# Kernel tuning notes

Hardware: AMD Instinct MI355X
Metric: run time of the kernel (lower is better)

The kernel has to match this reference:

```python
import jax, jax.numpy as jnp
import numpy as np

NB, NLOC, NALL, NNEI, A_SEL = 1, 512, 640, 96, 20
N_DIM, E_DIM, A_DIM, AXIS = 128, 64, 64, 4
EDGE_INFO = 2 * N_DIM + E_DIM          # 320
SYM = AXIS * (E_DIM + N_DIM)           # 768, cal_1_dim
ANGLE = A_DIM + N_DIM + 2 * E_DIM      # 320, angle_dim


def setup_inputs() -> dict:
    key = jax.random.key(0)
    ks = jax.random.split(key, 16)
    nrm = lambda k, sh, s=1.0: jax.random.normal(k, sh, dtype=jnp.float32) * s

    def lin(k, din, dout, s=0.05):
        k1, k2 = jax.random.split(k)
        return nrm(k1, (din, dout), s), nrm(k2, (dout,), s)

    inp = {}
    inp["g1_ext"] = nrm(ks[0], (NB, NALL, N_DIM))
    inp["g2"] = nrm(ks[1], (NB, NLOC, NNEI, E_DIM))
    inp["h2"] = nrm(ks[2], (NB, NLOC, NNEI, 3))
    inp["angle_embed"] = nrm(ks[3], (NB, NLOC, A_SEL, A_SEL, A_DIM))
    inp["sw"] = jax.random.uniform(ks[4], (NB, NLOC, NNEI), dtype=jnp.float32)
    inp["a_sw"] = jax.random.uniform(ks[5], (NB, NLOC, A_SEL), dtype=jnp.float32)
    inp["w_self"], inp["b_self"] = lin(ks[6], N_DIM, N_DIM)
    inp["w_proj"] = nrm(ks[7], (E_DIM, N_DIM), 0.05)  # proj_g1g2, bias=False
    inp["w_lin1"], inp["b_lin1"] = lin(ks[8], SYM, N_DIM)
    inp["w_edge1"], inp["b_edge1"] = lin(ks[9], EDGE_INFO, N_DIM)
    inp["w_lin2"], inp["b_lin2"] = lin(ks[10], EDGE_INFO, E_DIM)
    inp["w_ang"], inp["b_ang"] = lin(ks[11], ANGLE, A_DIM)
    inp["w_ga1"], inp["b_ga1"] = lin(ks[12], ANGLE, E_DIM)
    inp["w_ga2"], inp["b_ga2"] = lin(ks[13], E_DIM, E_DIM)
    inp["nlist"] = jax.random.randint(ks[14], (NB, NLOC, NNEI), 0, NALL)
    inp["nlist_mask"] = jnp.ones((NB, NLOC, NNEI), dtype=bool)
    inp["a_nlist_mask"] = jnp.ones((NB, NLOC, A_SEL), dtype=bool)
    return inp


def _sym_op(g, h2, mask, sw, axis):
    # symmetrization_op: _cal_hg (smooth, use_sqrt_nnei) followed by _cal_grrg
    # g: nb x nloc x nnei x d, h2: nb x nloc x nnei x 3
    g = jnp.where(mask[..., None], g, 0.0) * sw[..., None]
    inv = np.float32(1.0 / np.sqrt(g.shape[2]))
    hg = jnp.einsum('blnt,blnd->bltd', h2, g) * inv
    grrg = jnp.einsum('bltd,blta->blda', hg, hg[..., :axis])  # nb x nloc x d x axis
    return grrg.reshape(grrg.shape[0], grrg.shape[1], -1)


def reference(g1_ext, g2, h2, angle_embed, sw, a_sw,
              w_self, b_self, w_proj, w_lin1, b_lin1, w_edge1, b_edge1,
              w_lin2, b_lin2, w_ang, b_ang, w_ga1, b_ga1, w_ga2, b_ga2,
              nlist, nlist_mask, a_nlist_mask):
    act = jax.nn.silu
    nb, nloc, nnei, e_dim = g2.shape
    n_dim = g1_ext.shape[-1]
    a_sel = angle_embed.shape[2]
    g1 = g1_ext[:, :nloc]
    # _make_nei_g1: gather neighbor node features, nb x nloc x nnei x n_dim
    gg1 = jnp.take_along_axis(
        g1_ext, nlist.reshape(nb, nloc * nnei, 1), axis=1
    ).reshape(nb, nloc, nnei, n_dim)
    maskf = nlist_mask[..., None]
    swf = sw[..., None]

    g1_update = [g1]
    # node self mlp
    g1_update.append(act(g1 @ w_self + b_self))
    # conv update: masked+switched gg1 times projected g2, mean over nnei
    gg1_ms = jnp.where(maskf, gg1, 0.0) * swf
    g1_update.append(jnp.sum((g2 @ w_proj) * gg1_ms, axis=2) / np.float32(nnei))
    # symmetrized axis-neuron update
    sym = jnp.concatenate(
        [_sym_op(g2, h2, nlist_mask, sw, AXIS),
         _sym_op(gg1, h2, nlist_mask, sw, AXIS)], axis=-1)
    g1_update.append(act(sym @ w_lin1 + b_lin1))
    # edge info: [tiled g1, gg1, g2] -> 2*n_dim + e_dim
    edge_info = jnp.concatenate(
        [jnp.broadcast_to(g1[:, :, None, :], (nb, nloc, nnei, n_dim)), gg1, g2],
        axis=-1)
    g1_edge = act(edge_info @ w_edge1 + b_edge1) * swf
    g1_update.append(jnp.sum(g1_edge, axis=2) / np.float32(nnei))
    # res_avg
    g1_new = sum(g1_update) / np.float32(np.sqrt(len(g1_update)))

    g2_update = [g2, act(edge_info @ w_lin2 + b_lin2)]

    # angle branch: angle_dim = a_dim + n_dim + 2*e_dim
    g2a = jnp.where(a_nlist_mask[..., None], g2[:, :, :a_sel, :], 0.0)
    ang = jnp.concatenate([
        angle_embed,
        jnp.broadcast_to(g1[:, :, None, None, :], (nb, nloc, a_sel, a_sel, n_dim)),
        jnp.broadcast_to(g2a[:, :, :, None, :], (nb, nloc, a_sel, a_sel, e_dim)),
        jnp.broadcast_to(g2a[:, :, None, :, :], (nb, nloc, a_sel, a_sel, e_dim)),
    ], axis=-1)
    a_new = (angle_embed + act(ang @ w_ang + b_ang)) / np.float32(np.sqrt(2.0))

    # angle -> edge message, switch-weighted on both angle axes, mean over one axis
    ang_w = ang * a_sw[:, :, :, None, None] * a_sw[:, :, None, :, None]
    g2_ang = jnp.sum(act(ang_w @ w_ga1 + b_ga1), axis=3) / np.float32(a_sel)
    g2_ang_full = jnp.concatenate(
        [g2_ang, jnp.zeros((nb, nloc, nnei - a_sel, e_dim), g2.dtype)], axis=2)
    g2_update.append(act(g2_ang_full @ w_ga2 + b_ga2))
    g2_new = sum(g2_update) / np.float32(np.sqrt(len(g2_update)))

    return g1_new, g2_new, h2, a_new
```

## Files before the change

kernel.cpp:

```cpp
#include <hip/hip_runtime.h>
#include <hip/hip_bf16.h>

#define NLOC 512
#define NALL 640
#define NNEI 96
#define ASEL 20
#define NDIM 128
#define EDIM 64
#define ADIM 64

typedef short bf16x8 __attribute__((ext_vector_type(8)));
typedef float f32x4 __attribute__((ext_vector_type(4)));
typedef unsigned short ushort8 __attribute__((ext_vector_type(8)));
typedef unsigned short ushort4_t __attribute__((ext_vector_type(4)));

__device__ __forceinline__ unsigned short f2bf(float f) {
    unsigned int u = __float_as_uint(f);
    unsigned int r = (u + 0x7FFFu + ((u >> 16) & 1u)) >> 16;
    return (unsigned short)r;
}
__device__ __forceinline__ float bf2f(unsigned short u) {
    return __uint_as_float(((unsigned int)u) << 16);
}
__device__ __forceinline__ float silu(float x) { return x / (1.0f + __expf(-x)); }

__device__ __forceinline__ void cvt8_store(unsigned short* dst, const float* src) {
    float4 f0 = *(const float4*)src;
    float4 f1 = *(const float4*)(src + 4);
    ushort8 v;
    v[0] = f2bf(f0.x); v[1] = f2bf(f0.y); v[2] = f2bf(f0.z); v[3] = f2bf(f0.w);
    v[4] = f2bf(f1.x); v[5] = f2bf(f1.y); v[6] = f2bf(f1.z); v[7] = f2bf(f1.w);
    *(ushort8*)dst = v;
}

__global__ void prep_bt2(const float* __restrict__ w_ang, const float* __restrict__ w_ga1,
                         const float* __restrict__ w_edge1, const float* __restrict__ w_lin2,
                         const float* __restrict__ w_proj, const float* __restrict__ w_self,
                         unsigned short* __restrict__ bt_ae, unsigned short* __restrict__ bt_g2e,
                         unsigned short* __restrict__ bt_sm, unsigned short* __restrict__ bt_pij) {
    int idx = blockIdx.x * 256 + threadIdx.x;
    if (idx < 8192) {
        int k = idx & 63, n = idx >> 6;
        bt_ae[idx] = f2bf((n < 64) ? w_ang[k * 64 + n] : w_ga1[k * 64 + (n - 64)]);
    } else if (idx < 32768) {
        int id2 = idx - 8192;
        int k = id2 & 63, n = id2 >> 6;
        float v;
        if (n < 128)      v = w_edge1[(256 + k) * 128 + n];
        else if (n < 192) v = w_lin2[(256 + k) * 64 + (n - 128)];
        else if (n < 256) v = 0.0f;
        else              v = w_proj[k * 128 + (n - 256)];
        bt_g2e[id2] = f2bf(v);
    } else if (idx < 114688) {
        int id3 = idx - 32768;
        int k = id3 & 127, n = id3 >> 7;
        float v;
        if (n < 128)      v = w_edge1[k * 128 + n];
        else if (n < 192) v = w_lin2[k * 64 + (n - 128)];
        else if (n < 320) v = w_edge1[(128 + k) * 128 + (n - 192)];
        else if (n < 384) v = w_lin2[(128 + k) * 64 + (n - 320)];
        else if (n < 512) { int c = n - 384;
            v = (c < 64) ? w_ang[(64 + k) * 64 + c] : w_ga1[(64 + k) * 64 + (c - 64)]; }
        else              v = w_self[k * 128 + (n - 512)];
        bt_sm[id3] = f2bf(v);
    } else {
        int id4 = idx - 114688;
        int k = id4 & 63, n = id4 >> 6;
        float v;
        if (n < 128) v = (n < 64) ? w_ang[(192 + k) * 64 + n] : w_ga1[(192 + k) * 64 + (n - 64)];
        else { int c = n - 128;
            v = (c < 64) ? w_ang[(256 + k) * 64 + c] : w_ga1[(256 + k) * 64 + (c - 64)]; }
        bt_pij[id4] = f2bf(v);
    }
}

__global__ __launch_bounds__(256) void gemm_small(
    const float* __restrict__ g1_ext, const unsigned short* __restrict__ bt_sm,
    const float* __restrict__ b_self, float* __restrict__ P1a, float* __restrict__ g1self,
    float* __restrict__ E1, float* __restrict__ E2) {
    const int m0 = blockIdx.x * 128;
    const int ntile = blockIdx.y;
    __shared__ __align__(16) unsigned short Asl[128 * 136];
    __shared__ __align__(16) unsigned short Bsl[128 * 136];
    const int tid = threadIdx.x;
#pragma unroll
    for (int u = 0; u < 8; u++) {
        int g = tid + u * 256;
        int row = g >> 4, seg = g & 15;
        cvt8_store(&Asl[row * 136 + seg * 8], g1_ext + (m0 + row) * 128 + seg * 8);
        *(ushort8*)&Bsl[row * 136 + seg * 8] =
            *(const ushort8*)&bt_sm[(ntile * 128 + row) * 128 + seg * 8];
    }
    __syncthreads();
    const int lane = tid & 63, wid = tid >> 6;
    const int wr = wid >> 1, wc = wid & 1;
    const int r15 = lane & 15, kg = lane >> 4;
    f32x4 acc[4][4] = {};
#pragma unroll
    for (int h = 0; h < 4; h++) {
        bf16x8 afr[4], bfr[4];
#pragma unroll
        for (int mi = 0; mi < 4; mi++)
            afr[mi] = *(const bf16x8*)&Asl[(wr * 64 + mi * 16 + r15) * 136 + h * 32 + kg * 8];
#pragma unroll
        for (int ni = 0; ni < 4; ni++)
            bfr[ni] = *(const bf16x8*)&Bsl[(wc * 64 + ni * 16 + r15) * 136 + h * 32 + kg * 8];
#pragma unroll
        for (int mi = 0; mi < 4; mi++)
#pragma unroll
            for (int ni = 0; ni < 4; ni++)
                acc[mi][ni] = __builtin_amdgcn_mfma_f32_16x16x32_bf16(afr[mi], bfr[ni], acc[mi][ni], 0, 0, 0);
    }
#pragma unroll
    for (int mi = 0; mi < 4; mi++) {
        int rbase = m0 + wr * 64 + mi * 16 + kg * 4;
#pragma unroll
        for (int ni = 0; ni < 4; ni++) {
            int gc = ntile * 128 + wc * 64 + ni * 16 + r15;
#pragma unroll
            for (int t2 = 0; t2 < 4; t2++) {
                int a = rbase + t2;
                float z = acc[mi][ni][t2];
                if (gc < 192) { if (a < 512) E1[a * 192 + gc] = z; }
                else if (gc < 384) E2[a * 192 + (gc - 192)] = z;
                else if (gc < 512) { if (a < 512) P1a[a * 128 + (gc - 384)] = z; }
                else { if (a < 512) g1self[a * 128 + (gc - 512)] = silu(z + b_self[gc - 512]); }
            }
        }
    }
}

__global__ __launch_bounds__(256) void gemm_pij(
    const float* __restrict__ g2, const unsigned short* __restrict__ bt_pij,
    unsigned short* __restrict__ P_i, unsigned short* __restrict__ P_j) {
    const int m0 = blockIdx.x * 128;
    const int ntile = blockIdx.y;
    __shared__ __align__(16) unsigned short Asl[128 * 72];
    const int tid = threadIdx.x;
#pragma unroll
    for (int u = 0; u < 4; u++) {
        int g = tid + u * 256;
        int row = g >> 3, seg = g & 7;
        int li = m0 + row, l = li / 20, i = li - l * 20;
        cvt8_store(&Asl[row * 72 + seg * 8], g2 + (l * 96 + i) * 64 + seg * 8);
    }
    __syncthreads();
    const int lane = tid & 63, wid = tid >> 6;
    const int wr = wid >> 1, wc = wid & 1;
    const int r15 = lane & 15, kg = lane >> 4;
    f32x4 acc[4][4] = {};
#pragma unroll
    for (int h = 0; h < 2; h++) {
        bf16x8 afr[4], bfr[4];
#pragma unroll
        for (int mi = 0; mi < 4; mi++)
            afr[mi] = *(const bf16x8*)&Asl[(wr * 64 + mi * 16 + r15) * 72 + h * 32 + kg * 8];
#pragma unroll
        for (int ni = 0; ni < 4; ni++)
            bfr[ni] = *(const bf16x8*)&bt_pij[(ntile * 128 + wc * 64 + ni * 16 + r15) * 64 + h * 32 + kg * 8];
#pragma unroll
        for (int mi = 0; mi < 4; mi++)
#pragma unroll
            for (int ni = 0; ni < 4; ni++)
                acc[mi][ni] = __builtin_amdgcn_mfma_f32_16x16x32_bf16(afr[mi], bfr[ni], acc[mi][ni], 0, 0, 0);
    }
    unsigned short* Pout = (ntile == 0) ? P_i : P_j;
#pragma unroll
    for (int mi = 0; mi < 4; mi++) {
        int rbase = m0 + wr * 64 + mi * 16 + kg * 4;
#pragma unroll
        for (int ni = 0; ni < 4; ni++) {
            int c = wc * 64 + ni * 16 + r15;
#pragma unroll
            for (int t2 = 0; t2 < 4; t2++)
                Pout[(rbase + t2) * 128 + c] = f2bf(acc[mi][ni][t2]);
        }
    }
}

__global__ void k_sym(const float* __restrict__ g1_ext, const float* __restrict__ g2,
                      const float* __restrict__ h2, const float* __restrict__ sw,
                      const int* __restrict__ nlist, const float* __restrict__ w_lin1,
                      const float* __restrict__ b_lin1, float* __restrict__ term4) {
    int l = blockIdx.x, t = threadIdx.x;
    __shared__ float h2s[96 * 3];
    __shared__ float sws[96];
    __shared__ int nls[96];
    __shared__ float hg[3 * 192];
    __shared__ float symv[768];
    __shared__ float red[128];
    if (t < 96) { sws[t] = sw[l * 96 + t]; nls[t] = nlist[l * 96 + t]; }
    for (int p = t; p < 288; p += 256) h2s[p] = h2[l * 288 + p];
    __syncthreads();
    const float inv = 0.1020620726f;
    for (int p = t; p < 576; p += 256) {
        float acc = 0.0f;
        if (p < 192) {
            int tt = p >> 6, d = p & 63;
            for (int n = 0; n < 96; n++)
                acc += h2s[n * 3 + tt] * g2[(l * 96 + n) * 64 + d] * sws[n];
            hg[tt * 192 + d] = acc * inv;
        } else {
            int q = p - 192;
            int tt = q >> 7, d = q & 127;
            for (int n = 0; n < 96; n++)
                acc += h2s[n * 3 + tt] * g1_ext[nls[n] * 128 + d] * sws[n];
            hg[tt * 192 + 64 + d] = acc * inv;
        }
    }
    __syncthreads();
    for (int p = t; p < 768; p += 256) {
        float acc = 0.0f;
        if (p < 256) {
            int d = p >> 2, a = p & 3;
            for (int tt = 0; tt < 3; tt++) acc += hg[tt * 192 + d] * hg[tt * 192 + a];
        } else {
            int q = p - 256;
            int d = q >> 2, a = q & 3;
            for (int tt = 0; tt < 3; tt++) acc += hg[tt * 192 + 64 + d] * hg[tt * 192 + 64 + a];
        }
        symv[p] = acc;
    }
    __syncthreads();
    {
        int col = t & 127, half = t >> 7;
        float acc = 0.0f;
        int k0 = half * 384;
#pragma unroll 8
        for (int k = k0; k < k0 + 384; k++) acc += symv[k] * w_lin1[k * 128 + col];
        if (half) red[col] = acc;
        __syncthreads();
        if (!half) term4[l * 128 + col] = silu(acc + red[col] + b_lin1[col]);
    }
}

__global__ __launch_bounds__(256) void angle_main(
    const float* __restrict__ ae, const unsigned short* __restrict__ bt_ae,
    const float* __restrict__ P1a, const unsigned short* __restrict__ P_i,
    const unsigned short* __restrict__ P_j, const float* __restrict__ a_sw,
    const float* __restrict__ b_ang, const float* __restrict__ b_ga1,
    float* __restrict__ g2acc, float* __restrict__ a_new_out) {
    const int m0 = blockIdx.x * 128;
    __shared__ __align__(16) unsigned short Asl[128 * 72];
    const int tid = threadIdx.x;
#pragma unroll
    for (int u = 0; u < 4; u++) {
        int g = tid + u * 256;
        int row = g >> 3, seg = g & 7;
        cvt8_store(&Asl[row * 72 + seg * 8], ae + (m0 + row) * 64 + seg * 8);
    }
    __syncthreads();
    const int lane = tid & 63, wid = tid >> 6;
    const int wr = wid >> 1, wc = wid & 1;
    const int r15 = lane & 15, kg = lane >> 4;
    f32x4 acc[4][4] = {};
    if (wc == 0) {
#pragma unroll
        for (int h = 0; h < 2; h++) {
            bf16x8 afr[4], bfr[4];
#pragma unroll
            for (int mi = 0; mi < 4; mi++)
                afr[mi] = *(const bf16x8*)&Asl[(wr * 64 + mi * 16 + r15) * 72 + h * 32 + kg * 8];
#pragma unroll
            for (int ni = 0; ni < 4; ni++)
                bfr[ni] = *(const bf16x8*)&bt_ae[(ni * 16 + r15) * 64 + h * 32 + kg * 8];
#pragma unroll
            for (int mi = 0; mi < 4; mi++)
#pragma unroll
                for (int ni = 0; ni < 4; ni++)
                    acc[mi][ni] = __builtin_amdgcn_mfma_f32_16x16x32_bf16(bfr[ni], afr[mi], acc[mi][ni], 0, 0, 0);
        }
#pragma unroll
        for (int mi = 0; mi < 4; mi++) {
            int r = m0 + wr * 64 + mi * 16 + r15;
            int l = r / 400;
            int rem = r - l * 400;
            int i = rem / 20;
            int j = rem - i * 20;
            const float* p1b = P1a + l * 128;
            const unsigned short* pib = P_i + (l * 20 + i) * 128;
            const unsigned short* pjb = P_j + (l * 20 + j) * 128;
            int lr = r - m0;
#pragma unroll
            for (int ni = 0; ni < 4; ni++) {
                int n0 = ni * 16 + kg * 4;
                f32x4 p1v = *(const f32x4*)&p1b[n0];
                ushort4_t piv = *(const ushort4_t*)&pib[n0];
                ushort4_t pjv = *(const ushort4_t*)&pjb[n0];
                ushort4_t aev = *(const ushort4_t*)&Asl[lr * 72 + n0];
                f32x4 bbv = *(const f32x4*)&b_ang[n0];
                f32x4 outv;
#pragma unroll
                for (int t2 = 0; t2 < 4; t2++) {
                    float z = acc[mi][ni][t2] + p1v[t2] + bf2f(piv[t2]) + bf2f(pjv[t2]);
                    outv[t2] = (bf2f(aev[t2]) + silu(z + bbv[t2])) * 0.70710678f;
                }
                *(f32x4*)&a_new_out[r * 64 + n0] = outv;
            }
        }
    } else {
#pragma unroll
        for (int h = 0; h < 2; h++) {
            bf16x8 afr[4], bfr[4];
#pragma unroll
            for (int mi = 0; mi < 4; mi++)
                afr[mi] = *(const bf16x8*)&Asl[(wr * 64 + mi * 16 + r15) * 72 + h * 32 + kg * 8];
#pragma unroll
            for (int ni = 0; ni < 4; ni++)
                bfr[ni] = *(const bf16x8*)&bt_ae[(64 + ni * 16 + r15) * 64 + h * 32 + kg * 8];
#pragma unroll
            for (int mi = 0; mi < 4; mi++)
#pragma unroll
                for (int ni = 0; ni < 4; ni++)
                    acc[mi][ni] = __builtin_amdgcn_mfma_f32_16x16x32_bf16(afr[mi], bfr[ni], acc[mi][ni], 0, 0, 0);
        }
#pragma unroll
        for (int mi = 0; mi < 4; mi++) {
            int rbase = m0 + wr * 64 + mi * 16 + kg * 4;
            int l = rbase / 400;
            int rem = rbase - l * 400;
            int i = rem / 20;
            int j0 = rem - i * 20;
            const float* p1b = P1a + l * 128;
            const unsigned short* pib = P_i + (l * 20 + i) * 128;
            const unsigned short* pjb = P_j + l * 20 * 128;
            float swi = a_sw[l * 20 + i];
#pragma unroll
            for (int ni = 0; ni < 4; ni++) {
                int c = 64 + ni * 16 + r15;
                int cc = c - 64;
                float base = p1b[c] + bf2f(pib[c]);
                float bb = b_ga1[cc];
                float part = 0.0f;
#pragma unroll
                for (int t2 = 0; t2 < 4; t2++) {
                    int j = j0 + t2;
                    float z = acc[mi][ni][t2] + base + bf2f(pjb[j * 128 + c]);
                    float s = swi * a_sw[l * 20 + j];
                    part += silu(s * z + bb);
                }
                atomicAdd(&g2acc[(l * 20 + i) * 64 + cc], part);
            }
        }
    }
}

__global__ void k_f2(const float* __restrict__ g2ang_acc, const float* __restrict__ w_ga2,
                     const float* __restrict__ b_ga2, float* __restrict__ yga2) {
    int l = blockIdx.x, t = threadIdx.x;
    __shared__ float gs[20 * 64];
    for (int p = t; p < 1280; p += 256) gs[p] = g2ang_acc[l * 1280 + p] * 0.05f;
    __syncthreads();
    for (int p = t; p < 1280; p += 256) {
        int i = p >> 6, c = p & 63;
        float acc = b_ga2[c];
#pragma unroll 8
        for (int k = 0; k < 64; k++) acc += gs[i * 64 + k] * w_ga2[k * 64 + c];
        yga2[l * 1280 + p] = silu(acc);
    }
}

__global__ __launch_bounds__(256) void edge_main(
    const float* __restrict__ g1_ext, const float* __restrict__ g2, const float* __restrict__ sw,
    const int* __restrict__ nlist, const unsigned short* __restrict__ bt_g2e,
    const float* __restrict__ E1, const float* __restrict__ E2,
    const float* __restrict__ b_edge1, const float* __restrict__ b_lin2,
    const float* __restrict__ b_ga2, const float* __restrict__ yga2,
    float* __restrict__ g1_acc3, float* __restrict__ g1_acc5, float* __restrict__ g2_new_out) {
    const int m0 = blockIdx.x * 128;
    const int ntile = blockIdx.y;
    __shared__ __align__(16) unsigned short Asl[128 * 72];
    const int tid = threadIdx.x;
#pragma unroll
    for (int u = 0; u < 4; u++) {
        int g = tid + u * 256;
        int row = g >> 3, seg = g & 7;
        cvt8_store(&Asl[row * 72 + seg * 8], g2 + (m0 + row) * 64 + seg * 8);
    }
    __syncthreads();
    const int lane = tid & 63, wid = tid >> 6;
    const int wr = wid >> 1, wc = wid & 1;
    const int r15 = lane & 15, kg = lane >> 4;
    f32x4 acc[4][4] = {};
    if (ntile == 1) {
#pragma unroll
        for (int h = 0; h < 2; h++) {
            bf16x8 afr[4], bfr[4];
#pragma unroll
            for (int mi = 0; mi < 4; mi++)
                afr[mi] = *(const bf16x8*)&Asl[(wr * 64 + mi * 16 + r15) * 72 + h * 32 + kg * 8];
#pragma unroll
            for (int ni = 0; ni < 4; ni++)
                bfr[ni] = *(const bf16x8*)&bt_g2e[(128 + wc * 64 + ni * 16 + r15) * 64 + h * 32 + kg * 8];
#pragma unroll
            for (int mi = 0; mi < 4; mi++)
#pragma unroll
                for (int ni = 0; ni < 4; ni++)
                    acc[mi][ni] = __builtin_amdgcn_mfma_f32_16x16x32_bf16(bfr[ni], afr[mi], acc[mi][ni], 0, 0, 0);
        }
        if (wc == 0) {
#pragma unroll
            for (int mi = 0; mi < 4; mi++) {
                int r = m0 + wr * 64 + mi * 16 + r15;
                int l = r / 96;
                int nn = r - l * 96;
                const float* e1 = E1 + l * 192 + 128;
                const float* e2 = E2 + nlist[r] * 192 + 128;
                bool hasyg = (nn < ASEL);
                const float* yg = yga2 + (l * 20 + nn) * 64;
                int lr = r - m0;
#pragma unroll
                for (int ni = 0; ni < 4; ni++) {
                    int n0 = ni * 16 + kg * 4;
                    f32x4 e1v = *(const f32x4*)&e1[n0];
                    f32x4 e2v = *(const f32x4*)&e2[n0];
                    f32x4 bbv = *(const f32x4*)&b_lin2[n0];
                    f32x4 bg2 = *(const f32x4*)&b_ga2[n0];
                    ushort4_t g2v = *(const ushort4_t*)&Asl[lr * 72 + n0];
                    f32x4 outv;
#pragma unroll
                    for (int t2 = 0; t2 < 4; t2++) {
                        float z = acc[mi][ni][t2] + e1v[t2] + e2v[t2];
                        float y = silu(z + bbv[t2]);
                        float ygv = hasyg ? yg[n0 + t2] : silu(bg2[t2]);
                        outv[t2] = (bf2f(g2v[t2]) + y + ygv) * 0.57735027f;
                    }
                    *(f32x4*)&g2_new_out[r * 64 + n0] = outv;
                }
            }
        }
    } else {
#pragma unroll
        for (int h = 0; h < 2; h++) {
            bf16x8 afr[4], bfr[4];
#pragma unroll
            for (int mi = 0; mi < 4; mi++)
                afr[mi] = *(const bf16x8*)&Asl[(wr * 64 + mi * 16 + r15) * 72 + h * 32 + kg * 8];
#pragma unroll
            for (int ni = 0; ni < 4; ni++)
                bfr[ni] = *(const bf16x8*)&bt_g2e[(ntile * 128 + wc * 64 + ni * 16 + r15) * 64 + h * 32 + kg * 8];
#pragma unroll
            for (int mi = 0; mi < 4; mi++)
#pragma unroll
                for (int ni = 0; ni < 4; ni++)
                    acc[mi][ni] = __builtin_amdgcn_mfma_f32_16x16x32_bf16(afr[mi], bfr[ni], acc[mi][ni], 0, 0, 0);
        }
#pragma unroll
        for (int mi = 0; mi < 4; mi++) {
            int rbase = m0 + wr * 64 + mi * 16 + kg * 4;
            int l = rbase / 96;
#pragma unroll
            for (int ni = 0; ni < 4; ni++) {
                int c = wc * 64 + ni * 16 + r15;
                if (ntile == 0) {
                    float e1 = E1[l * 192 + c];
                    float bb = b_edge1[c];
                    float part = 0.0f;
#pragma unroll
                    for (int t2 = 0; t2 < 4; t2++) {
                        int r = rbase + t2;
                        float z = acc[mi][ni][t2] + e1 + E2[nlist[r] * 192 + c];
                        part += silu(z + bb) * sw[r];
                    }
                    atomicAdd(&g1_acc5[l * 128 + c], part);
                } else {
                    float part = 0.0f;
#pragma unroll
                    for (int t2 = 0; t2 < 4; t2++) {
                        int r = rbase + t2;
                        part += acc[mi][ni][t2] * g1_ext[nlist[r] * 128 + c] * sw[r];
                    }
                    atomicAdd(&g1_acc3[l * 128 + c], part);
                }
            }
        }
    }
}

__global__ void k_f1(const float* __restrict__ g1_ext, const float* __restrict__ g1self,
                     const float* __restrict__ acc3, const float* __restrict__ term4,
                     const float* __restrict__ acc5, float* __restrict__ out_g1) {
    int idx = blockIdx.x * 256 + threadIdx.x;
    float v = g1_ext[idx] + g1self[idx] + acc3[idx] * (1.0f / 96.0f) + term4[idx] +
              acc5[idx] * (1.0f / 96.0f);
    out_g1[idx] = v * 0.4472135955f;
}

extern "C" void kernel_launch(void* const* d_in, const int* in_sizes, int n_in,
                              void* d_out, int out_size, void* d_ws, size_t ws_size,
                              hipStream_t stream) {
    if (n_in < 22 || in_sizes[0] != 81920 || in_sizes[3] != 13107200) return;
    const float* g1_ext = (const float*)d_in[0];
    const float* g2     = (const float*)d_in[1];
    const float* h2     = (const float*)d_in[2];
    const float* ae     = (const float*)d_in[3];
    const float* sw     = (const float*)d_in[4];
    const float* a_sw   = (const float*)d_in[5];
    const float* w_self = (const float*)d_in[6];
    const float* b_self = (const float*)d_in[7];
    const float* w_proj = (const float*)d_in[8];
    const float* w_lin1 = (const float*)d_in[9];
    const float* b_lin1 = (const float*)d_in[10];
    const float* w_edge1= (const float*)d_in[11];
    const float* b_edge1= (const float*)d_in[12];
    const float* w_lin2 = (const float*)d_in[13];
    const float* b_lin2 = (const float*)d_in[14];
    const float* w_ang  = (const float*)d_in[15];
    const float* b_ang  = (const float*)d_in[16];
    const float* w_ga1  = (const float*)d_in[17];
    const float* b_ga1  = (const float*)d_in[18];
    const float* w_ga2  = (const float*)d_in[19];
    const float* b_ga2  = (const float*)d_in[20];
    const int*   nlist  = (const int*)d_in[21];

    float* ws = (float*)d_ws;
    unsigned short* bt_ae  = (unsigned short*)(ws);
    unsigned short* bt_g2e = (unsigned short*)(ws + 4096);
    unsigned short* bt_sm  = (unsigned short*)(ws + 16384);
    unsigned short* bt_pij = (unsigned short*)(ws + 57344);
    float* P1a    = ws + 65536;
    float* E1     = ws + 131072;
    float* E2     = ws + 229376;
    unsigned short* P_i = (unsigned short*)(ws + 352256);
    unsigned short* P_j = (unsigned short*)(ws + 1007616);
    float* g1self = ws + 1662976;
    float* term4  = ws + 1728512;
    float* yga2   = ws + 1794048;
    float* acc3   = ws + 2449408;
    float* acc5   = ws + 2514944;
    float* g2acc  = ws + 2580480;
    if (ws_size < (size_t)3235840 * sizeof(float)) return;

    float* out = (float*)d_out;
    float* out_g1 = out;
    float* out_g2 = out + 65536;
    float* out_h2 = out + 3211264;
    float* out_an = out + 3358720;

    hipMemsetAsync(acc3, 0, (65536 + 65536 + 655360) * sizeof(float), stream);

    prep_bt2<<<512, 256, 0, stream>>>(w_ang, w_ga1, w_edge1, w_lin2, w_proj, w_self,
                                      bt_ae, bt_g2e, bt_sm, bt_pij);
    gemm_small<<<dim3(5, 5), 256, 0, stream>>>(g1_ext, bt_sm, b_self, P1a, g1self, E1, E2);
    gemm_pij<<<dim3(80, 2), 256, 0, stream>>>(g2, bt_pij, P_i, P_j);
    k_sym<<<512, 256, 0, stream>>>(g1_ext, g2, h2, sw, nlist, w_lin1, b_lin1, term4);
    angle_main<<<1600, 256, 0, stream>>>(ae, bt_ae, P1a, P_i, P_j, a_sw, b_ang, b_ga1,
                                         g2acc, out_an);
    k_f2<<<512, 256, 0, stream>>>(g2acc, w_ga2, b_ga2, yga2);
    edge_main<<<dim3(384, 3), 256, 0, stream>>>(g1_ext, g2, sw, nlist, bt_g2e, E1, E2,
                                                b_edge1, b_lin2, b_ga2, yga2,
                                                acc3, acc5, out_g2);
    k_f1<<<256, 256, 0, stream>>>(g1_ext, g1self, acc3, term4, acc5, out_g1);
    hipMemcpyAsync(out_h2, h2, 147456 * sizeof(float), hipMemcpyDeviceToDevice, stream);
}
```

Baseline: 180.9 us.

## Rebalance angle_main warps across both outputs and add transposed P_j layout

angle_main previously split warps so half computed the a_new output and half the g2 message. Now each warp handles 32 rows for both output halves, so every warp carries the same load. gemm_pij additionally writes a transposed copy of P_j so the message epilogue can read four consecutive j values as one vector load instead of strided scalar loads. The ntile==1 path of edge_main gets the same row split, which removes the idle wc==1 epilogue warps. The cost is an extra scattered transposed store in gemm_pij and more workspace.

```diff
diff --git a/kernel.cpp b/kernel.cpp
--- a/kernel.cpp
+++ b/kernel.cpp
@@ -132,7 +132,8 @@
 
 __global__ __launch_bounds__(256) void gemm_pij(
     const float* __restrict__ g2, const unsigned short* __restrict__ bt_pij,
-    unsigned short* __restrict__ P_i, unsigned short* __restrict__ P_j) {
+    unsigned short* __restrict__ P_i, unsigned short* __restrict__ P_j,
+    unsigned short* __restrict__ P_jT) {
     const int m0 = blockIdx.x * 128;
     const int ntile = blockIdx.y;
     __shared__ __align__(16) unsigned short Asl[128 * 72];
@@ -172,8 +173,15 @@
         for (int ni = 0; ni < 4; ni++) {
             int c = wc * 64 + ni * 16 + r15;
 #pragma unroll
-            for (int t2 = 0; t2 < 4; t2++)
-                Pout[(rbase + t2) * 128 + c] = f2bf(acc[mi][ni][t2]);
+            for (int t2 = 0; t2 < 4; t2++) {
+                unsigned short v = f2bf(acc[mi][ni][t2]);
+                int li = rbase + t2;
+                Pout[li * 128 + c] = v;
+                if (ntile == 1) {
+                    int l = li / 20, j = li - l * 20;
+                    P_jT[(l * 128 + c) * 20 + j] = v;
+                }
+            }
         }
     }
 }
@@ -237,7 +245,8 @@
 __global__ __launch_bounds__(256) void angle_main(
     const float* __restrict__ ae, const unsigned short* __restrict__ bt_ae,
     const float* __restrict__ P1a, const unsigned short* __restrict__ P_i,
-    const unsigned short* __restrict__ P_j, const float* __restrict__ a_sw,
+    const unsigned short* __restrict__ P_j, const unsigned short* __restrict__ P_jT,
+    const float* __restrict__ a_sw,
     const float* __restrict__ b_ang, const float* __restrict__ b_ga1,
     float* __restrict__ g2acc, float* __restrict__ a_new_out) {
     const int m0 = blockIdx.x * 128;
@@ -251,96 +260,81 @@
     }
     __syncthreads();
     const int lane = tid & 63, wid = tid >> 6;
-    const int wr = wid >> 1, wc = wid & 1;
     const int r15 = lane & 15, kg = lane >> 4;
-    f32x4 acc[4][4] = {};
-    if (wc == 0) {
-#pragma unroll
-        for (int h = 0; h < 2; h++) {
-            bf16x8 afr[4], bfr[4];
-#pragma unroll
-            for (int mi = 0; mi < 4; mi++)
-                afr[mi] = *(const bf16x8*)&Asl[(wr * 64 + mi * 16 + r15) * 72 + h * 32 + kg * 8];
-#pragma unroll
-            for (int ni = 0; ni < 4; ni++)
-                bfr[ni] = *(const bf16x8*)&bt_ae[(ni * 16 + r15) * 64 + h * 32 + kg * 8];
-#pragma unroll
-            for (int mi = 0; mi < 4; mi++)
-#pragma unroll
-                for (int ni = 0; ni < 4; ni++)
-                    acc[mi][ni] = __builtin_amdgcn_mfma_f32_16x16x32_bf16(bfr[ni], afr[mi], acc[mi][ni], 0, 0, 0);
-        }
-#pragma unroll
-        for (int mi = 0; mi < 4; mi++) {
-            int r = m0 + wr * 64 + mi * 16 + r15;
-            int l = r / 400;
-            int rem = r - l * 400;
-            int i = rem / 20;
-            int j = rem - i * 20;
-            const float* p1b = P1a + l * 128;
-            const unsigned short* pib = P_i + (l * 20 + i) * 128;
-            const unsigned short* pjb = P_j + (l * 20 + j) * 128;
-            int lr = r - m0;
+    f32x4 accA[2][4] = {};
+    f32x4 accB[2][4] = {};
+#pragma unroll
+    for (int h = 0; h < 2; h++) {
+        bf16x8 afr[2], bfrA[4], bfrB[4];
+#pragma unroll
+        for (int mi = 0; mi < 2; mi++)
+            afr[mi] = *(const bf16x8*)&Asl[(wid * 32 + mi * 16 + r15) * 72 + h * 32 + kg * 8];
+#pragma unroll
+        for (int ni = 0; ni < 4; ni++) {
+            bfrA[ni] = *(const bf16x8*)&bt_ae[(ni * 16 + r15) * 64 + h * 32 + kg * 8];
+            bfrB[ni] = *(const bf16x8*)&bt_ae[(64 + ni * 16 + r15) * 64 + h * 32 + kg * 8];
+        }
+#pragma unroll
+        for (int mi = 0; mi < 2; mi++)
 #pragma unroll
             for (int ni = 0; ni < 4; ni++) {
-                int n0 = ni * 16 + kg * 4;
-                f32x4 p1v = *(const f32x4*)&p1b[n0];
-                ushort4_t piv = *(const ushort4_t*)&pib[n0];
-                ushort4_t pjv = *(const ushort4_t*)&pjb[n0];
-                ushort4_t aev = *(const ushort4_t*)&Asl[lr * 72 + n0];
-                f32x4 bbv = *(const f32x4*)&b_ang[n0];
-                f32x4 outv;
-#pragma unroll
-                for (int t2 = 0; t2 < 4; t2++) {
-                    float z = acc[mi][ni][t2] + p1v[t2] + bf2f(piv[t2]) + bf2f(pjv[t2]);
-                    outv[t2] = (bf2f(aev[t2]) + silu(z + bbv[t2])) * 0.70710678f;
-                }
-                *(f32x4*)&a_new_out[r * 64 + n0] = outv;
-            }
-        }
-    } else {
-#pragma unroll
-        for (int h = 0; h < 2; h++) {
-            bf16x8 afr[4], bfr[4];
-#pragma unroll
-            for (int mi = 0; mi < 4; mi++)
-                afr[mi] = *(const bf16x8*)&Asl[(wr * 64 + mi * 16 + r15) * 72 + h * 32 + kg * 8];
-#pragma unroll
-            for (int ni = 0; ni < 4; ni++)
-                bfr[ni] = *(const bf16x8*)&bt_ae[(64 + ni * 16 + r15) * 64 + h * 32 + kg * 8];
-#pragma unroll
-            for (int mi = 0; mi < 4; mi++)
-#pragma unroll
-                for (int ni = 0; ni < 4; ni++)
-                    acc[mi][ni] = __builtin_amdgcn_mfma_f32_16x16x32_bf16(afr[mi], bfr[ni], acc[mi][ni], 0, 0, 0);
-        }
-#pragma unroll
-        for (int mi = 0; mi < 4; mi++) {
-            int rbase = m0 + wr * 64 + mi * 16 + kg * 4;
-            int l = rbase / 400;
-            int rem = rbase - l * 400;
-            int i = rem / 20;
-            int j0 = rem - i * 20;
-            const float* p1b = P1a + l * 128;
-            const unsigned short* pib = P_i + (l * 20 + i) * 128;
-            const unsigned short* pjb = P_j + l * 20 * 128;
-            float swi = a_sw[l * 20 + i];
-#pragma unroll
-            for (int ni = 0; ni < 4; ni++) {
-                int c = 64 + ni * 16 + r15;
-                int cc = c - 64;
-                float base = p1b[c] + bf2f(pib[c]);
-                float bb = b_ga1[cc];
-                float part = 0.0f;
-#pragma unroll
-                for (int t2 = 0; t2 < 4; t2++) {
-                    int j = j0 + t2;
-                    float z = acc[mi][ni][t2] + base + bf2f(pjb[j * 128 + c]);
-                    float s = swi * a_sw[l * 20 + j];
-                    part += silu(s * z + bb);
-                }
-                atomicAdd(&g2acc[(l * 20 + i) * 64 + cc], part);
-            }
+                accA[mi][ni] = __builtin_amdgcn_mfma_f32_16x16x32_bf16(bfrA[ni], afr[mi], accA[mi][ni], 0, 0, 0);
+                accB[mi][ni] = __builtin_amdgcn_mfma_f32_16x16x32_bf16(afr[mi], bfrB[ni], accB[mi][ni], 0, 0, 0);
+            }
+    }
+#pragma unroll
+    for (int mi = 0; mi < 2; mi++) {
+        int r = m0 + wid * 32 + mi * 16 + r15;
+        int l = r / 400;
+        int rem = r - l * 400;
+        int i = rem / 20;
+        int j = rem - i * 20;
+        const float* p1b = P1a + l * 128;
+        const unsigned short* pib = P_i + (l * 20 + i) * 128;
+        const unsigned short* pjb = P_j + (l * 20 + j) * 128;
+        int lr = r - m0;
+#pragma unroll
+        for (int ni = 0; ni < 4; ni++) {
+            int n0 = ni * 16 + kg * 4;
+            f32x4 p1v = *(const f32x4*)&p1b[n0];
+            ushort4_t piv = *(const ushort4_t*)&pib[n0];
+            ushort4_t pjv = *(const ushort4_t*)&pjb[n0];
+            ushort4_t aev = *(const ushort4_t*)&Asl[lr * 72 + n0];
+            f32x4 bbv = *(const f32x4*)&b_ang[n0];
+            f32x4 outv;
+#pragma unroll
+            for (int t2 = 0; t2 < 4; t2++) {
+                float z = accA[mi][ni][t2] + p1v[t2] + bf2f(piv[t2]) + bf2f(pjv[t2]);
+                outv[t2] = (bf2f(aev[t2]) + silu(z + bbv[t2])) * 0.70710678f;
+            }
+            *(f32x4*)&a_new_out[r * 64 + n0] = outv;
+        }
+    }
+#pragma unroll
+    for (int mi = 0; mi < 2; mi++) {
+        int rbase = m0 + wid * 32 + mi * 16 + kg * 4;
+        int l = rbase / 400;
+        int rem = rbase - l * 400;
+        int i = rem / 20;
+        int j0 = rem - i * 20;
+        const float* p1b = P1a + l * 128;
+        const unsigned short* pib = P_i + (l * 20 + i) * 128;
+        float swi = a_sw[l * 20 + i];
+        f32x4 swjv = *(const f32x4*)&a_sw[l * 20 + j0];
+#pragma unroll
+        for (int ni = 0; ni < 4; ni++) {
+            int c = 64 + ni * 16 + r15;
+            int cc = c - 64;
+            float base = p1b[c] + bf2f(pib[c]);
+            float bb = b_ga1[cc];
+            ushort4_t pjtv = *(const ushort4_t*)&P_jT[(l * 128 + c) * 20 + j0];
+            float part = 0.0f;
+#pragma unroll
+            for (int t2 = 0; t2 < 4; t2++) {
+                float z = accB[mi][ni][t2] + base + bf2f(pjtv[t2]);
+                part += silu(swi * swjv[t2] * z + bb);
+            }
+            atomicAdd(&g2acc[(l * 20 + i) * 64 + cc], part);
         }
     }
 }
@@ -379,57 +373,56 @@
     }
     __syncthreads();
     const int lane = tid & 63, wid = tid >> 6;
-    const int wr = wid >> 1, wc = wid & 1;
     const int r15 = lane & 15, kg = lane >> 4;
-    f32x4 acc[4][4] = {};
     if (ntile == 1) {
+        f32x4 acc[2][4] = {};
 #pragma unroll
         for (int h = 0; h < 2; h++) {
-            bf16x8 afr[4], bfr[4];
-#pragma unroll
-            for (int mi = 0; mi < 4; mi++)
-                afr[mi] = *(const bf16x8*)&Asl[(wr * 64 + mi * 16 + r15) * 72 + h * 32 + kg * 8];
+            bf16x8 afr[2], bfr[4];
+#pragma unroll
+            for (int mi = 0; mi < 2; mi++)
+                afr[mi] = *(const bf16x8*)&Asl[(wid * 32 + mi * 16 + r15) * 72 + h * 32 + kg * 8];
 #pragma unroll
             for (int ni = 0; ni < 4; ni++)
-                bfr[ni] = *(const bf16x8*)&bt_g2e[(128 + wc * 64 + ni * 16 + r15) * 64 + h * 32 + kg * 8];
-#pragma unroll
-            for (int mi = 0; mi < 4; mi++)
+                bfr[ni] = *(const bf16x8*)&bt_g2e[(128 + ni * 16 + r15) * 64 + h * 32 + kg * 8];
+#pragma unroll
+            for (int mi = 0; mi < 2; mi++)
 #pragma unroll
                 for (int ni = 0; ni < 4; ni++)
                     acc[mi][ni] = __builtin_amdgcn_mfma_f32_16x16x32_bf16(bfr[ni], afr[mi], acc[mi][ni], 0, 0, 0);
         }
-        if (wc == 0) {
-#pragma unroll
-            for (int mi = 0; mi < 4; mi++) {
-                int r = m0 + wr * 64 + mi * 16 + r15;
-                int l = r / 96;
-                int nn = r - l * 96;
-                const float* e1 = E1 + l * 192 + 128;
-                const float* e2 = E2 + nlist[r] * 192 + 128;
-                bool hasyg = (nn < ASEL);
-                const float* yg = yga2 + (l * 20 + nn) * 64;
-                int lr = r - m0;
-#pragma unroll
-                for (int ni = 0; ni < 4; ni++) {
-                    int n0 = ni * 16 + kg * 4;
-                    f32x4 e1v = *(const f32x4*)&e1[n0];
-                    f32x4 e2v = *(const f32x4*)&e2[n0];
-                    f32x4 bbv = *(const f32x4*)&b_lin2[n0];
-                    f32x4 bg2 = *(const f32x4*)&b_ga2[n0];
-                    ushort4_t g2v = *(const ushort4_t*)&Asl[lr * 72 + n0];
-                    f32x4 outv;
-#pragma unroll
-                    for (int t2 = 0; t2 < 4; t2++) {
-                        float z = acc[mi][ni][t2] + e1v[t2] + e2v[t2];
-                        float y = silu(z + bbv[t2]);
-                        float ygv = hasyg ? yg[n0 + t2] : silu(bg2[t2]);
-                        outv[t2] = (bf2f(g2v[t2]) + y + ygv) * 0.57735027f;
-                    }
-                    *(f32x4*)&g2_new_out[r * 64 + n0] = outv;
+#pragma unroll
+        for (int mi = 0; mi < 2; mi++) {
+            int r = m0 + wid * 32 + mi * 16 + r15;
+            int l = r / 96;
+            int nn = r - l * 96;
+            const float* e1 = E1 + l * 192 + 128;
+            const float* e2 = E2 + nlist[r] * 192 + 128;
+            bool hasyg = (nn < ASEL);
+            const float* yg = yga2 + (l * 20 + nn) * 64;
+            int lr = r - m0;
+#pragma unroll
+            for (int ni = 0; ni < 4; ni++) {
+                int n0 = ni * 16 + kg * 4;
+                f32x4 e1v = *(const f32x4*)&e1[n0];
+                f32x4 e2v = *(const f32x4*)&e2[n0];
+                f32x4 bbv = *(const f32x4*)&b_lin2[n0];
+                f32x4 bg2 = *(const f32x4*)&b_ga2[n0];
+                ushort4_t g2v = *(const ushort4_t*)&Asl[lr * 72 + n0];
+                f32x4 outv;
+#pragma unroll
+                for (int t2 = 0; t2 < 4; t2++) {
+                    float z = acc[mi][ni][t2] + e1v[t2] + e2v[t2];
+                    float y = silu(z + bbv[t2]);
+                    float ygv = hasyg ? yg[n0 + t2] : silu(bg2[t2]);
+                    outv[t2] = (bf2f(g2v[t2]) + y + ygv) * 0.57735027f;
                 }
+                *(f32x4*)&g2_new_out[r * 64 + n0] = outv;
             }
         }
     } else {
+        const int wr = wid >> 1, wc = wid & 1;
+        f32x4 acc[4][4] = {};
 #pragma unroll
         for (int h = 0; h < 2; h++) {
             bf16x8 afr[4], bfr[4];
@@ -529,7 +522,8 @@
     float* acc3   = ws + 2449408;
     float* acc5   = ws + 2514944;
     float* g2acc  = ws + 2580480;
-    if (ws_size < (size_t)3235840 * sizeof(float)) return;
+    unsigned short* P_jT = (unsigned short*)(ws + 3235840);
+    if (ws_size < (size_t)3563520 * sizeof(float)) return;
 
     float* out = (float*)d_out;
     float* out_g1 = out;
@@ -542,9 +536,9 @@
     prep_bt2<<<512, 256, 0, stream>>>(w_ang, w_ga1, w_edge1, w_lin2, w_proj, w_self,
                                       bt_ae, bt_g2e, bt_sm, bt_pij);
     gemm_small<<<dim3(5, 5), 256, 0, stream>>>(g1_ext, bt_sm, b_self, P1a, g1self, E1, E2);
-    gemm_pij<<<dim3(80, 2), 256, 0, stream>>>(g2, bt_pij, P_i, P_j);
+    gemm_pij<<<dim3(80, 2), 256, 0, stream>>>(g2, bt_pij, P_i, P_j, P_jT);
     k_sym<<<512, 256, 0, stream>>>(g1_ext, g2, h2, sw, nlist, w_lin1, b_lin1, term4);
-    angle_main<<<1600, 256, 0, stream>>>(ae, bt_ae, P1a, P_i, P_j, a_sw, b_ang, b_ga1,
+    angle_main<<<1600, 256, 0, stream>>>(ae, bt_ae, P1a, P_i, P_j, P_jT, a_sw, b_ang, b_ga1,
                                          g2acc, out_an);
     k_f2<<<512, 256, 0, stream>>>(g2acc, w_ga2, b_ga2, yga2);
     edge_main<<<dim3(384, 3), 256, 0, stream>>>(g1_ext, g2, sw, nlist, bt_g2e, E1, E2,
```

Result: no change. 178.4 us (-1.4%).
